# Optimization experiments

Hardware: AMD Instinct MI355X
Metric: run time of the kernel (lower is better)

Reference implementation:

```python
import jax, jax.numpy as jnp
import numpy as np

SEQ, H, VOCAB = 2048, 1024, 32000

def setup_inputs() -> dict:
    key = jax.random.key(0)
    ks = jax.random.split(key, 13)
    s = lambda k, shape, fan: jax.random.normal(k, shape, dtype=jnp.float32) / np.sqrt(fan)
    return {
        "word_input": jax.random.randint(ks[0], (1,), 0, VOCAB, dtype=jnp.int64),
        "last_context": s(ks[1], (1, H), H),
        "last_hidden": s(ks[2], (1, H), H),
        "encoder_outputs": s(ks[3], (SEQ, H), H),
        "emb": s(ks[4], (VOCAB, H), H),
        "W_ih": s(ks[5], (4 * H, 2 * H), 2 * H),
        "W_hh": s(ks[6], (4 * H, H), H),
        "b_ih": s(ks[7], (4 * H,), H),
        "b_hh": s(ks[8], (4 * H,), H),
        "Wa": s(ks[9], (H, H), H),
        "ba": s(ks[10], (H,), H),
        "Wl": s(ks[11], (VOCAB, 2 * H), 2 * H),
        "bl": s(ks[12], (VOCAB,), 2 * H),
    }

def reference(word_input, last_context, last_hidden, encoder_outputs,
              emb, W_ih, W_hh, b_ih, b_hh, Wa, ba, Wl, bl):
    # embedding lookup (batch=1, single step): [H]
    x = emb[word_input[0]]
    # rnn_input = cat(embedded, last_context): [2H]
    inp = jnp.concatenate([x, last_context[0]])
    h0 = last_hidden[0]
    c0 = jnp.zeros_like(h0)
    # single LSTM step, PyTorch gate order (i, f, g, o)
    gates = W_ih @ inp + b_ih + W_hh @ h0 + b_hh  # [4H]
    i_g, f_g, g_g, o_g = jnp.split(gates, 4)
    c = jax.nn.sigmoid(f_g) * c0 + jax.nn.sigmoid(i_g) * jnp.tanh(g_g)
    h = jax.nn.sigmoid(o_g) * jnp.tanh(c)  # lstm_output, [H]
    # Bahdanau-style scores: dot(h, Wa @ enc_i + ba) for each position (vectorized)
    energies = (encoder_outputs @ Wa.T + ba) @ h  # [SEQ]
    attn_w = jax.nn.softmax(energies)
    context = attn_w @ encoder_outputs  # [H]
    logits = Wl @ jnp.concatenate([h, context]) + bl  # [VOCAB]
    out = jax.nn.log_softmax(logits)
    return out[None, :]  # [1, VOCAB]
```

## Files before the change

### kernel.cpp

```cpp
#include <hip/hip_runtime.h>
#include <hip/hip_bf16.h>
#include <math.h>

#define SEQ   2048
#define H     1024
#define VOCAB 32000

__device__ inline float4 ld4(const float* p) { return *reinterpret_cast<const float4*>(p); }
__device__ inline float dot4(float4 a, float4 b) { return a.x*b.x + a.y*b.y + a.z*b.z + a.w*b.w; }
__device__ inline float sigmoidf(float x) { return 1.f / (1.f + expf(-x)); }

__device__ inline void omerge(float& m, float& s, float m2, float s2) {
    if (m2 > m) { s = s * __expf(m - m2) + s2; m = m2; }
    else if (s2 != 0.f) { s += s2 * __expf(m2 - m); }
}
__device__ inline float waveSum(float v) {
#pragma unroll
    for (int off = 32; off > 0; off >>= 1) v += __shfl_down(v, off, 64);
    return v;
}
__device__ inline void waveOmerge(float& m, float& s) {
#pragma unroll
    for (int off = 32; off > 0; off >>= 1) {
        float m2 = __shfl_down(m, off, 64), ss = __shfl_down(s, off, 64);
        omerge(m, s, m2, ss);
    }
}

__global__ __launch_bounds__(256) void k_lstm(
        const float* __restrict__ emb, const float* __restrict__ lctx,
        const float* __restrict__ h0,  const float* __restrict__ W_ih,
        const float* __restrict__ W_hh, const float* __restrict__ b_ih,
        const float* __restrict__ b_hh, const int* __restrict__ widx,
        float* __restrict__ h_out, float* __restrict__ u_zero,
        float* __restrict__ ctx_zero) {
    const int j = blockIdx.x, t = threadIdx.x;
    const int wid = t >> 6, lane = t & 63;
    if (j == 0) for (int k = t; k < H; k += 256) u_zero[k] = 0.f;
    if (j == 1) for (int k = t; k < H; k += 256) ctx_zero[k] = 0.f;

    const int w = widx[0];
    const float* embrow = emb + (size_t)w * H;
    const int ri = j, rg = j + 2 * H, ro = j + 3 * H;
    const float* wi_i = W_ih + (size_t)ri * (2 * H);
    const float* wi_g = W_ih + (size_t)rg * (2 * H);
    const float* wi_o = W_ih + (size_t)ro * (2 * H);
    const float* wh_i = W_hh + (size_t)ri * H;
    const float* wh_g = W_hh + (size_t)rg * H;
    const float* wh_o = W_hh + (size_t)ro * H;

    float ai = 0.f, ag = 0.f, ao = 0.f;
    { int e = t*4; float4 x = ld4(embrow+e);
      ai += dot4(ld4(wi_i+e),x); ag += dot4(ld4(wi_g+e),x); ao += dot4(ld4(wi_o+e),x); }
    { int e = t*4; float4 x = ld4(lctx+e);
      ai += dot4(ld4(wi_i+H+e),x); ag += dot4(ld4(wi_g+H+e),x); ao += dot4(ld4(wi_o+H+e),x); }
    { int e = t*4; float4 x = ld4(h0+e);
      ai += dot4(ld4(wh_i+e),x); ag += dot4(ld4(wh_g+e),x); ao += dot4(ld4(wh_o+e),x); }
    ai = waveSum(ai); ag = waveSum(ag); ao = waveSum(ao);
    __shared__ float lds[12];
    if (lane == 0) { lds[wid*3] = ai; lds[wid*3+1] = ag; lds[wid*3+2] = ao; }
    __syncthreads();
    if (t == 0) {
        float gi = 0.f, gg = 0.f, go = 0.f;
        for (int q = 0; q < 4; ++q) { gi += lds[q*3]; gg += lds[q*3+1]; go += lds[q*3+2]; }
        gi += b_ih[ri] + b_hh[ri];
        gg += b_ih[rg] + b_hh[rg];
        go += b_ih[ro] + b_hh[ro];
        float c = sigmoidf(gi) * tanhf(gg);
        h_out[j] = sigmoidf(go) * tanhf(c);
    }
}

__global__ __launch_bounds__(256) void k_wa(
        const float* __restrict__ Wa, const float* __restrict__ h,
        float* __restrict__ u) {
    const int k = blockIdx.x * 256 + threadIdx.x;
    const int j0 = blockIdx.y * 32;
    float acc = 0.f;
#pragma unroll 8
    for (int j = j0; j < j0 + 32; ++j) acc += Wa[(size_t)j * H + k] * h[j];
    atomicAdd(&u[k], acc);
}

__global__ __launch_bounds__(256) void k_energy(
        const float* __restrict__ enc, const float* __restrict__ u,
        float* __restrict__ energ, float2* __restrict__ part_e) {
    const int t = threadIdx.x, wid = t >> 6, lane = t & 63;
    const int row = blockIdx.x * 4 + wid;
    const float* er = enc + (size_t)row * H;
    float acc = 0.f;
#pragma unroll
    for (int it = 0; it < 4; ++it) { int e = it*256 + lane*4; acc += dot4(ld4(er+e), ld4(u+e)); }
    acc = waveSum(acc);
    __shared__ float se[4];
    if (lane == 0) { energ[row] = acc; se[wid] = acc; }
    __syncthreads();
    if (t == 0) {
        float m = fmaxf(fmaxf(se[0], se[1]), fmaxf(se[2], se[3]));
        float s = __expf(se[0]-m) + __expf(se[1]-m) + __expf(se[2]-m) + __expf(se[3]-m);
        part_e[blockIdx.x] = make_float2(m, s);
    }
}

__global__ __launch_bounds__(256) void k_ctx(
        const float* __restrict__ enc, const float* __restrict__ energ,
        const float2* __restrict__ part_e, float* __restrict__ ctx) {
    const int t = threadIdx.x, wid = t >> 6, lane = t & 63;
    __shared__ float2 s2[4];
    __shared__ float sh[64];

    float2 a = part_e[t], b = part_e[t + 256];
    float m = a.x, s = a.y;
    omerge(m, s, b.x, b.y);
    waveOmerge(m, s);
    if (lane == 0) s2[wid] = make_float2(m, s);
    __syncthreads();
    float M = s2[0].x, S = s2[0].y;
#pragma unroll
    for (int q = 1; q < 4; ++q) omerge(M, S, s2[q].x, s2[q].y);
    const float invS = 1.f / S;

    const int j0 = (blockIdx.x >> 2) * 64;
    __syncthreads();
    if (t < 64) sh[t] = __expf(energ[j0 + t] - M) * invS;
    __syncthreads();
    const int k = (blockIdx.x & 3) * 256 + t;
    float acc = 0.f;
#pragma unroll 8
    for (int jj = 0; jj < 64; ++jj) acc += sh[jj] * enc[(size_t)(j0 + jj) * H + k];
    atomicAdd(&ctx[k], acc);
}

__global__ __launch_bounds__(256) void k_logits(
        const float* __restrict__ Wl, const float* __restrict__ vcat,
        const float* __restrict__ bl, float* __restrict__ logits,
        float2* __restrict__ part_l) {
    const int t = threadIdx.x, wid = t >> 6, lane = t & 63;
    const int gw = blockIdx.x * 4 + wid;

    float4 xv[8];
#pragma unroll
    for (int q = 0; q < 8; ++q) xv[q] = ld4(vcat + q * 256 + lane * 4);

    float lm = -INFINITY, ls = 0.f;
#pragma unroll
    for (int rr = 0; rr < 4; ++rr) {
        const int row = gw * 4 + rr;
        const float* wr = Wl + (size_t)row * (2 * H);
        float acc = 0.f;
#pragma unroll
        for (int q = 0; q < 8; ++q)
            acc += dot4(ld4(wr + q * 256 + lane * 4), xv[q]);
        acc = waveSum(acc);
        if (lane == 0) {
            float v = acc + bl[row];
            logits[row] = v;
            omerge(lm, ls, v, 1.f);
        }
    }
    __shared__ float2 s2[4];
    if (lane == 0) s2[wid] = make_float2(lm, ls);
    __syncthreads();
    if (t == 0) {
        float M = s2[0].x, S = s2[0].y;
#pragma unroll
        for (int q = 1; q < 4; ++q) omerge(M, S, s2[q].x, s2[q].y);
        part_l[blockIdx.x] = make_float2(M, S);
    }
}

__global__ __launch_bounds__(256) void k_final(
        const float* __restrict__ logits, const float2* __restrict__ part_l,
        float* __restrict__ out) {
    const int t = threadIdx.x, wid = t >> 6, lane = t & 63;
    __shared__ float2 s2[4];
    float m = -INFINITY, s = 0.f;
    for (int i = t; i < 2000; i += 256) {
        float2 p = part_l[i];
        omerge(m, s, p.x, p.y);
    }
    waveOmerge(m, s);
    if (lane == 0) s2[wid] = make_float2(m, s);
    __syncthreads();
    float M = s2[0].x, S = s2[0].y;
#pragma unroll
    for (int q = 1; q < 4; ++q) omerge(M, S, s2[q].x, s2[q].y);
    const float lse = M + logf(S);
    const int i = blockIdx.x * 256 + t;
    out[i] = logits[i] - lse;
}

extern "C" void kernel_launch(void* const* d_in, const int* in_sizes, int n_in,
                              void* d_out, int out_size, void* d_ws, size_t ws_size,
                              hipStream_t stream) {
    const int*   widx = (const int*)d_in[0];
    const float* lctx = (const float*)d_in[1];
    const float* h0   = (const float*)d_in[2];
    const float* enc  = (const float*)d_in[3];
    const float* emb  = (const float*)d_in[4];
    const float* W_ih = (const float*)d_in[5];
    const float* W_hh = (const float*)d_in[6];
    const float* b_ih = (const float*)d_in[7];
    const float* b_hh = (const float*)d_in[8];
    const float* Wa   = (const float*)d_in[9];
    const float* Wl   = (const float*)d_in[11];
    const float* bl   = (const float*)d_in[12];
    float* out = (float*)d_out;
    float* ws  = (float*)d_ws;

    float*  h      = ws;
    float*  ctx    = ws + 1024;
    float*  u      = ws + 2048;
    float*  energ  = ws + 3072;
    float2* part_e = (float2*)(ws + 5120);
    float2* part_l = (float2*)(ws + 6144);
    float*  logits = ws + 10240;

    k_lstm  <<<1024, 256, 0, stream>>>(emb, lctx, h0, W_ih, W_hh, b_ih, b_hh, widx, h, u, ctx);
    k_wa    <<<dim3(4, 32), 256, 0, stream>>>(Wa, h, u);
    k_energy<<<512, 256, 0, stream>>>(enc, u, energ, part_e);
    k_ctx   <<<128, 256, 0, stream>>>(enc, energ, part_e, ctx);
    k_logits<<<2000, 256, 0, stream>>>(Wl, ws , bl, logits, part_l);
    k_final <<<125, 256, 0, stream>>>(logits, part_l, out);
}
```

Measured before the change: 74.82 us.

## Fuse decoder step into one persistent kernel with atomic-flag grid barriers

```diff
diff --git a/kernel.cpp b/kernel.cpp
--- a/kernel.cpp
+++ b/kernel.cpp
@@ -5,6 +5,8 @@
 #define SEQ   2048
 #define H     1024
 #define VOCAB 32000
+#define GRID2 2048
+#define NTHR  256
 
 __device__ inline float4 ld4(const float* p) { return *reinterpret_cast<const float4*>(p); }
 __device__ inline float dot4(float4 a, float4 b) { return a.x*b.x + a.y*b.y + a.z*b.z + a.w*b.w; }
@@ -26,6 +28,222 @@
         omerge(m, s, m2, ss);
     }
 }
+
+__device__ inline void blockSignal(unsigned* f) {
+    __syncthreads();
+    if (threadIdx.x == 0) {
+        __threadfence();
+        __hip_atomic_fetch_add(f, 1u, __ATOMIC_RELEASE, __HIP_MEMORY_SCOPE_AGENT);
+    }
+}
+__device__ inline void blockWait(unsigned* f, unsigned target) {
+    if (threadIdx.x == 0) {
+        while (__hip_atomic_load(f, __ATOMIC_ACQUIRE, __HIP_MEMORY_SCOPE_AGENT) < target)
+            __builtin_amdgcn_s_sleep(4);
+        __threadfence();
+    }
+    __syncthreads();
+}
+
+
+__global__ __launch_bounds__(NTHR) void k_init(float* __restrict__ ws) {
+    const int t = threadIdx.x;
+    unsigned* fl = (unsigned*)ws;
+    if (t < 96) fl[t] = 0u;
+    float* u   = ws + 2144;
+    float* ctx = ws + 1120;
+    for (int k = t; k < H; k += NTHR) { u[k] = 0.f; ctx[k] = 0.f; }
+}
+
+__global__ __launch_bounds__(NTHR, 8) void k_main(
+        const float* __restrict__ emb,  const float* __restrict__ lctx,
+        const float* __restrict__ h0,   const float* __restrict__ W_ih,
+        const float* __restrict__ W_hh, const float* __restrict__ b_ih,
+        const float* __restrict__ b_hh, const int* __restrict__ widx,
+        const float* __restrict__ enc,  const float* __restrict__ Wa,
+        const float* __restrict__ Wl,   const float* __restrict__ bl,
+        float* __restrict__ ws, float* __restrict__ out) {
+    const int bid = blockIdx.x, t = threadIdx.x;
+    const int wid = t >> 6, lane = t & 63;
+
+    unsigned* f_h   = (unsigned*)ws + 0;
+    unsigned* f_u   = (unsigned*)ws + 16;
+    unsigned* f_e   = (unsigned*)ws + 32;
+    unsigned* f_ctx = (unsigned*)ws + 48;
+    unsigned* f_l   = (unsigned*)ws + 64;
+    float*  h      = ws + 96;
+    float*  ctx    = ws + 1120;
+    float*  u      = ws + 2144;
+    float*  energ  = ws + 3168;
+    float2* part_e = (float2*)(ws + 5216);
+    float2* part_l = (float2*)(ws + 5728);
+
+    __shared__ float  lg[12];
+    __shared__ float  shh[16];
+    __shared__ float  se[8];
+    __shared__ float  shw[32];
+    __shared__ float2 s2[4];
+
+    if (bid >= 1024) {
+        const int j = bid - 1024;
+        const int w = widx[0];
+        const float* xe = emb + (size_t)w * H;
+        const float* wi = W_ih + (size_t)j * (2 * H);
+        const float* wg = W_ih + (size_t)(j + 2 * H) * (2 * H);
+        const float* wo = W_ih + (size_t)(j + 3 * H) * (2 * H);
+        const float* vi = W_hh + (size_t)j * H;
+        const float* vg = W_hh + (size_t)(j + 2 * H) * H;
+        const float* vo = W_hh + (size_t)(j + 3 * H) * H;
+        const int e = t * 4;
+        float4 x0 = ld4(xe + e), x1 = ld4(lctx + e), x2 = ld4(h0 + e);
+        float ai = dot4(ld4(wi + e), x0) + dot4(ld4(wi + H + e), x1) + dot4(ld4(vi + e), x2);
+        float ag = dot4(ld4(wg + e), x0) + dot4(ld4(wg + H + e), x1) + dot4(ld4(vg + e), x2);
+        float ao = dot4(ld4(wo + e), x0) + dot4(ld4(wo + H + e), x1) + dot4(ld4(vo + e), x2);
+        ai = waveSum(ai); ag = waveSum(ag); ao = waveSum(ao);
+        if (lane == 0) { lg[wid*3] = ai; lg[wid*3+1] = ag; lg[wid*3+2] = ao; }
+        __syncthreads();
+        if (t == 0) {
+            float gi = 0.f, gg = 0.f, go = 0.f;
+            for (int q = 0; q < 4; ++q) { gi += lg[q*3]; gg += lg[q*3+1]; go += lg[q*3+2]; }
+            gi += b_ih[j] + b_hh[j];
+            gg += b_ih[j + 2*H] + b_hh[j + 2*H];
+            go += b_ih[j + 3*H] + b_hh[j + 3*H];
+            float c = sigmoidf(gi) * tanhf(gg);
+            h[j] = sigmoidf(go) * tanhf(c);
+        }
+        blockSignal(f_h);
+    }
+
+    blockWait(f_h, 1024);
+
+    if (bid < 256) {
+        {
+            const int rg = bid >> 2, kb = bid & 3;
+            if (t < 16) shh[t] = h[rg * 16 + t];
+            __syncthreads();
+            const int k = kb * 256 + t;
+            float acc = 0.f;
+#pragma unroll
+            for (int jj = 0; jj < 16; ++jj)
+                acc += Wa[(size_t)(rg * 16 + jj) * H + k] * shh[jj];
+            atomicAdd(&u[k], acc);
+            blockSignal(f_u);
+            blockWait(f_u, 256);
+        }
+        {
+#pragma unroll
+            for (int rr = 0; rr < 2; ++rr) {
+                const int row = bid * 8 + wid * 2 + rr;
+                const float* er = enc + (size_t)row * H;
+                float acc = 0.f;
+#pragma unroll
+                for (int it = 0; it < 4; ++it) {
+                    const int e = it * 256 + lane * 4;
+                    acc += dot4(ld4(er + e), ld4(u + e));
+                }
+                acc = waveSum(acc);
+                if (lane == 0) { energ[row] = acc; se[wid * 2 + rr] = acc; }
+            }
+            __syncthreads();
+            if (t == 0) {
+                float m = -INFINITY, s = 0.f;
+                for (int q = 0; q < 8; ++q) omerge(m, s, se[q], 1.f);
+                part_e[bid] = make_float2(m, s);
+            }
+            blockSignal(f_e);
+            blockWait(f_e, 256);
+        }
+        {
+            float2 p = part_e[t];
+            float m = p.x, s = p.y;
+            waveOmerge(m, s);
+            if (lane == 0) s2[wid] = make_float2(m, s);
+            __syncthreads();
+            float M = s2[0].x, S = s2[0].y;
+#pragma unroll
+            for (int q = 1; q < 4; ++q) omerge(M, S, s2[q].x, s2[q].y);
+            const float invS = 1.f / S;
+            const int rg = bid >> 2, kb = bid & 3;
+            __syncthreads();
+            if (t < 32) shw[t] = __expf(energ[rg * 32 + t] - M) * invS;
+            __syncthreads();
+            const int k = kb * 256 + t;
+            float acc = 0.f;
+#pragma unroll
+            for (int jj = 0; jj < 32; ++jj)
+                acc += shw[jj] * enc[(size_t)(rg * 32 + jj) * H + k];
+            atomicAdd(&ctx[k], acc);
+            blockSignal(f_ctx);
+        }
+        if (bid < 125) {
+            blockWait(f_l, 1792);
+            float m = -INFINITY, s = 0.f;
+            for (int i = t; i < 1792; i += NTHR) {
+                float2 p = part_l[i];
+                omerge(m, s, p.x, p.y);
+            }
+            waveOmerge(m, s);
+            __syncthreads();
+            if (lane == 0) s2[wid] = make_float2(m, s);
+            __syncthreads();
+            float M = s2[0].x, S = s2[0].y;
+#pragma unroll
+            for (int q = 1; q < 4; ++q) omerge(M, S, s2[q].x, s2[q].y);
+            const float lse = M + logf(S);
+            const int i = bid * 256 + t;
+            out[i] = out[i] - lse;
+        }
+    } else {
+        const int gwS = (bid - 256) * 4 + wid;
+        const int NR = (gwS < 3328) ? 5 : 4;
+        float4 xv[4];
+#pragma unroll
+        for (int q = 0; q < 4; ++q) xv[q] = ld4(h + q * 256 + lane * 4);
+        float acc[5] = {0.f, 0.f, 0.f, 0.f, 0.f};
+#pragma unroll
+        for (int rr = 0; rr < 5; ++rr) {
+            if (rr < NR) {
+                const float* wr = Wl + (size_t)(gwS + 7168 * rr) * (2 * H);
+                float a = 0.f;
+#pragma unroll
+                for (int q = 0; q < 4; ++q)
+                    a += dot4(ld4(wr + q * 256 + lane * 4), xv[q]);
+                acc[rr] = a;
+            }
+        }
+        blockWait(f_ctx, 256);
+#pragma unroll
+        for (int q = 0; q < 4; ++q) xv[q] = ld4(ctx + q * 256 + lane * 4);
+        float lm = -INFINITY, ls = 0.f;
+#pragma unroll
+        for (int rr = 0; rr < 5; ++rr) {
+            if (rr < NR) {
+                const int r = gwS + 7168 * rr;
+                const float* wr = Wl + (size_t)r * (2 * H) + H;
+                float a = acc[rr];
+#pragma unroll
+                for (int q = 0; q < 4; ++q)
+                    a += dot4(ld4(wr + q * 256 + lane * 4), xv[q]);
+                a = waveSum(a);
+                if (lane == 0) {
+                    float v = a + bl[r];
+                    out[r] = v;
+                    omerge(lm, ls, v, 1.f);
+                }
+            }
+        }
+        if (lane == 0) s2[wid] = make_float2(lm, ls);
+        __syncthreads();
+        if (t == 0) {
+            float M = s2[0].x, S = s2[0].y;
+#pragma unroll
+            for (int q = 1; q < 4; ++q) omerge(M, S, s2[q].x, s2[q].y);
+            part_l[bid - 256] = make_float2(M, S);
+        }
+        blockSignal(f_l);
+    }
+}
+
 
 __global__ __launch_bounds__(256) void k_lstm(
         const float* __restrict__ emb, const float* __restrict__ lctx,
@@ -38,7 +256,6 @@
     const int wid = t >> 6, lane = t & 63;
     if (j == 0) for (int k = t; k < H; k += 256) u_zero[k] = 0.f;
     if (j == 1) for (int k = t; k < H; k += 256) ctx_zero[k] = 0.f;
-
     const int w = widx[0];
     const float* embrow = emb + (size_t)w * H;
     const int ri = j, rg = j + 2 * H, ro = j + 3 * H;
@@ -48,7 +265,6 @@
     const float* wh_i = W_hh + (size_t)ri * H;
     const float* wh_g = W_hh + (size_t)rg * H;
     const float* wh_o = W_hh + (size_t)ro * H;
-
     float ai = 0.f, ag = 0.f, ao = 0.f;
     { int e = t*4; float4 x = ld4(embrow+e);
       ai += dot4(ld4(wi_i+e),x); ag += dot4(ld4(wi_g+e),x); ao += dot4(ld4(wi_o+e),x); }
@@ -108,7 +324,6 @@
     const int t = threadIdx.x, wid = t >> 6, lane = t & 63;
     __shared__ float2 s2[4];
     __shared__ float sh[64];
-
     float2 a = part_e[t], b = part_e[t + 256];
     float m = a.x, s = a.y;
     omerge(m, s, b.x, b.y);
@@ -119,7 +334,6 @@
 #pragma unroll
     for (int q = 1; q < 4; ++q) omerge(M, S, s2[q].x, s2[q].y);
     const float invS = 1.f / S;
-
     const int j0 = (blockIdx.x >> 2) * 64;
     __syncthreads();
     if (t < 64) sh[t] = __expf(energ[j0 + t] - M) * invS;
@@ -137,11 +351,9 @@
         float2* __restrict__ part_l) {
     const int t = threadIdx.x, wid = t >> 6, lane = t & 63;
     const int gw = blockIdx.x * 4 + wid;
-
     float4 xv[8];
 #pragma unroll
     for (int q = 0; q < 8; ++q) xv[q] = ld4(vcat + q * 256 + lane * 4);
-
     float lm = -INFINITY, ls = 0.f;
 #pragma unroll
     for (int rr = 0; rr < 4; ++rr) {
@@ -208,18 +420,30 @@
     float* out = (float*)d_out;
     float* ws  = (float*)d_ws;
 
-    float*  h      = ws;
-    float*  ctx    = ws + 1024;
-    float*  u      = ws + 2048;
-    float*  energ  = ws + 3072;
-    float2* part_e = (float2*)(ws + 5120);
-    float2* part_l = (float2*)(ws + 6144);
-    float*  logits = ws + 10240;
-
-    k_lstm  <<<1024, 256, 0, stream>>>(emb, lctx, h0, W_ih, W_hh, b_ih, b_hh, widx, h, u, ctx);
-    k_wa    <<<dim3(4, 32), 256, 0, stream>>>(Wa, h, u);
-    k_energy<<<512, 256, 0, stream>>>(enc, u, energ, part_e);
-    k_ctx   <<<128, 256, 0, stream>>>(enc, energ, part_e, ctx);
-    k_logits<<<2000, 256, 0, stream>>>(Wl, ws , bl, logits, part_l);
-    k_final <<<125, 256, 0, stream>>>(logits, part_l, out);
-}
+    int occ = 0, nCU = 0, dev = 0;
+    hipGetDevice(&dev);
+    hipDeviceGetAttribute(&nCU, hipDeviceAttributeMultiprocessorCount, dev);
+    hipError_t oe = hipOccupancyMaxActiveBlocksPerMultiprocessor(
+        &occ, (const void*)k_main, NTHR, 0);
+    const bool persistent_ok = (oe == hipSuccess) && ((long)occ * nCU >= GRID2);
+
+    if (persistent_ok) {
+        k_init<<<1, NTHR, 0, stream>>>(ws);
+        k_main<<<GRID2, NTHR, 0, stream>>>(emb, lctx, h0, W_ih, W_hh, b_ih,
+                                           b_hh, widx, enc, Wa, Wl, bl, ws, out);
+    } else {
+        float*  h      = ws;
+        float*  ctx    = ws + 1024;
+        float*  u      = ws + 2048;
+        float*  energ  = ws + 3072;
+        float2* part_e = (float2*)(ws + 5120);
+        float2* part_l = (float2*)(ws + 6144);
+        float*  logits = ws + 10240;
+        k_lstm  <<<1024, 256, 0, stream>>>(emb, lctx, h0, W_ih, W_hh, b_ih, b_hh, widx, h, u, ctx);
+        k_wa    <<<dim3(4, 32), 256, 0, stream>>>(Wa, h, u);
+        k_energy<<<512, 256, 0, stream>>>(enc, u, energ, part_e);
+        k_ctx   <<<128, 256, 0, stream>>>(enc, energ, part_e, ctx);
+        k_logits<<<2000, 256, 0, stream>>>(Wl, ws , bl, logits, part_l);
+        k_final <<<125, 256, 0, stream>>>(logits, part_l, out);
+    }
+}
```

Measured after the change: 72.98 us. 2.5% less time.
